# Kernel tuning notes

Hardware: AMD Instinct MI355X
Metric: run time of the kernel (lower is better)

The kernel has to match this reference:

```python
import jax, jax.numpy as jnp
import numpy as np

B, V, N, H, C_OUT = 16, 8192, 2048, 128, 7


def setup_inputs() -> dict:
    key = jax.random.key(0)
    ks = jax.random.split(key, 5)
    return {
        "verts": jax.random.normal(ks[0], (B, V, 3), jnp.float32) * 10.0,
        "coords_ca": jax.random.normal(ks[1], (B, N, 3), jnp.float32) * 10.0,
        "feats": jax.random.normal(ks[2], (B, N, H), jnp.float32),
        "W1": jax.random.normal(ks[3], (H, H), jnp.float32) / np.sqrt(H),
        "b1": jnp.zeros((H,), jnp.float32),
        "W2": jax.random.normal(ks[4], (H, C_OUT), jnp.float32) / np.sqrt(H),
        "b2": jnp.zeros((C_OUT,), jnp.float32),
    }


def reference(verts, coords_ca, feats, W1, b1, W2, b2):
    # Per-graph: nearest-CA match for every surface vertex (cdist + argmin),
    # then sum over the UNIQUE set of matched residues (torch: processed[min_indices.unique()].sum(-2)).
    # Equivalent jit-friendly form: hit-mask over residues, masked sum.
    def per_graph(v, c, f):
        # squared euclidean distances [V, N]; argmin is invariant to the sqrt
        d = (jnp.sum(v * v, -1)[:, None]
             - 2.0 * (v @ c.T)
             + jnp.sum(c * c, -1)[None, :])
        mi = jnp.argmin(d, axis=1)                       # [V] nearest residue per vertex
        hit = jnp.zeros((c.shape[0],), f.dtype).at[mi].add(1.0)
        mask = (hit > 0).astype(f.dtype)                 # [N] residue selected at least once
        return jnp.einsum('nh,n->h', f, mask)            # sum over unique selected residues

    pooled = jax.vmap(per_graph)(verts, coords_ca, feats)  # [B, H]
    # top_net (Dropout is identity in eval)
    h = jax.nn.relu(pooled @ W1 + b1)
    return h @ W2 + b2                                    # [B, 7]
```

## Files before the change

kernel.cpp:

```cpp
#include <hip/hip_runtime.h>
#include <hip/hip_bf16.h>

#define B_GR   16
#define V_PTS  8192
#define N_RES  2048
#define H_DIM  128
#define C_OUT  7
#define SEGS   16

#define NSPLIT 16
#define NL     (N_RES / NSPLIT)
#define VPT    8
#define VBLK   (256 * VPT)
#define VBLKS  (V_PTS / VBLK)

__global__ __launch_bounds__(256, 4) void k_argmin(const float* __restrict__ verts,
                                                   const float* __restrict__ coords,
                                                   unsigned long long* __restrict__ mi64) {
    __shared__ float4 sc[NL];
    const int b  = blockIdx.x / (VBLKS * NSPLIT);
    const int r  = blockIdx.x % (VBLKS * NSPLIT);
    const int vb = r / NSPLIT;
    const int ns = r % NSPLIT;

    const float* cbase = coords + ((size_t)b * N_RES + ns * NL) * 3;
    if (threadIdx.x < NL) {
        const int i = threadIdx.x;
        float x = cbase[i * 3 + 0];
        float y = cbase[i * 3 + 1];
        float z = cbase[i * 3 + 2];
        float csq = __fadd_rn(__fadd_rn(__fmul_rn(x, x), __fmul_rn(y, y)), __fmul_rn(z, z));
        sc[i] = make_float4(x, y, z, csq);
    }
    __syncthreads();

    const int vbase = vb * VBLK + threadIdx.x;
    const float* vp = verts + (size_t)b * V_PTS * 3;

    float vx[VPT], vy[VPT], vz[VPT], vsq[VPT], best[VPT];
    int bi[VPT];
#pragma unroll
    for (int k = 0; k < VPT; ++k) {
        const int v = vbase + k * 256;
        vx[k] = vp[v * 3 + 0];
        vy[k] = vp[v * 3 + 1];
        vz[k] = vp[v * 3 + 2];
        vsq[k] = __fadd_rn(__fadd_rn(__fmul_rn(vx[k], vx[k]), __fmul_rn(vy[k], vy[k])),
                           __fmul_rn(vz[k], vz[k]));
        best[k] = 3.402823466e+38f;
        bi[k] = 0;
    }

#pragma unroll 2
    for (int n = 0; n < NL; ++n) {
        const float4 c = sc[n];
#pragma unroll
        for (int k = 0; k < VPT; ++k) {
            float dot = __fadd_rn(__fadd_rn(__fmul_rn(vx[k], c.x), __fmul_rn(vy[k], c.y)),
                                  __fmul_rn(vz[k], c.z));
            float d = __fadd_rn(fmaf(-2.0f, dot, vsq[k]), c.w);
            bool m = d < best[k];
            best[k] = m ? d : best[k];
            bi[k]   = m ? n : bi[k];
        }
    }

#pragma unroll
    for (int k = 0; k < VPT; ++k) {
        unsigned int bits = __float_as_uint(best[k]);
        unsigned int key  = bits ^ (unsigned int)(((int)bits >> 31) | 0x80000000);
        unsigned long long packed =
            ((unsigned long long)key << 32) | (unsigned int)(ns * NL + bi[k]);
        atomicMin(&mi64[(size_t)b * V_PTS + vbase + k * 256], packed);
    }
}

__global__ __launch_bounds__(256) void k_pool(const unsigned long long* __restrict__ mi64,
                                              const float* __restrict__ feats,
                                              float* __restrict__ partial) {
    __shared__ float msk[N_RES];
    __shared__ float4 red[8][32];
    const int b   = blockIdx.x >> 4;
    const int seg = blockIdx.x & (SEGS - 1);

    for (int i = threadIdx.x; i < N_RES; i += 256) msk[i] = 0.0f;
    __syncthreads();

    const unsigned long long* mb = mi64 + (size_t)b * V_PTS;
    for (int v = threadIdx.x; v < V_PTS; v += 256)
        msk[(unsigned int)mb[v]] = 1.0f;
    __syncthreads();

    const int q = threadIdx.x & 31;
    const int s = threadIdx.x >> 5;
    const int n0 = seg * (N_RES / SEGS);
    const float4* fb4 = (const float4*)(feats + ((size_t)b * N_RES + n0) * H_DIM);

    float4 acc = make_float4(0.f, 0.f, 0.f, 0.f);
#pragma unroll
    for (int n = 0; n < N_RES / SEGS / 8; ++n) {
        const int nn = s + n * 8;
        const float m = msk[n0 + nn];
        const float4 f = fb4[(size_t)nn * 32 + q];
        acc.x = fmaf(f.x, m, acc.x);
        acc.y = fmaf(f.y, m, acc.y);
        acc.z = fmaf(f.z, m, acc.z);
        acc.w = fmaf(f.w, m, acc.w);
    }
    red[s][q] = acc;
    __syncthreads();

    if (s == 0) {
        float4 t = acc;
#pragma unroll
        for (int i = 1; i < 8; ++i) {
            t.x += red[i][q].x; t.y += red[i][q].y;
            t.z += red[i][q].z; t.w += red[i][q].w;
        }
        ((float4*)partial)[((size_t)b * SEGS + seg) * 32 + q] = t;
    }
}

__global__ __launch_bounds__(128) void k_mlp(const float* __restrict__ partial,
                                             const float* __restrict__ W1,
                                             const float* __restrict__ b1,
                                             const float* __restrict__ W2,
                                             const float* __restrict__ b2,
                                             float* __restrict__ out) {
    __shared__ float pooled[H_DIM];
    __shared__ float h1[H_DIM];
    const int b = blockIdx.x;
    const int j = threadIdx.x;

    float s = 0.0f;
#pragma unroll
    for (int g = 0; g < SEGS; ++g)
        s += partial[((size_t)b * SEGS + g) * H_DIM + j];
    pooled[j] = s;
    __syncthreads();

    float acc = b1[j];
#pragma unroll 8
    for (int hh = 0; hh < H_DIM; ++hh)
        acc = fmaf(pooled[hh], W1[hh * H_DIM + j], acc);
    h1[j] = fmaxf(acc, 0.0f);
    __syncthreads();

    if (j < C_OUT) {
        float o = b2[j];
#pragma unroll 8
        for (int hh = 0; hh < H_DIM; ++hh)
            o = fmaf(h1[hh], W2[hh * C_OUT + j], o);
        out[(size_t)b * C_OUT + j] = o;
    }
}

extern "C" void kernel_launch(void* const* d_in, const int* in_sizes, int n_in,
                              void* d_out, int out_size, void* d_ws, size_t ws_size,
                              hipStream_t stream) {
    const float* verts  = (const float*)d_in[0];
    const float* coords = (const float*)d_in[1];
    const float* feats  = (const float*)d_in[2];
    const float* W1     = (const float*)d_in[3];
    const float* b1     = (const float*)d_in[4];
    const float* W2     = (const float*)d_in[5];
    const float* b2     = (const float*)d_in[6];
    float* out = (float*)d_out;

    unsigned long long* mi64 = (unsigned long long*)d_ws;
    float* partial = (float*)((char*)d_ws + (size_t)B_GR * V_PTS * 8);

    hipMemsetAsync(mi64, 0xFF, (size_t)B_GR * V_PTS * 8, stream);
    k_argmin<<<B_GR * VBLKS * NSPLIT, 256, 0, stream>>>(verts, coords, mi64);
    k_pool  <<<B_GR * SEGS,           256, 0, stream>>>(mi64, feats, partial);
    k_mlp   <<<B_GR,                  128, 0, stream>>>(partial, W1, b1, W2, b2, out);
}
```

Baseline: 150.8 us.

## Use packed FP32 math in argmin and fuse pooling with MLP via last-block counter

The argmin inner loop now works on pairs of vertices using v_pk_mul/add/fma_f32 inline asm, halving the VALU instruction count for the distance computation while keeping the separate rounding of the unfused reference. The pool and MLP kernels are merged: each pooling block increments a per-graph global counter, and the last block to finish reads all partials and runs the MLP. This removes one kernel launch, at the cost of a threadfence and an atomic per block, and relies on the counter resetting itself correctly between calls.

```diff
diff --git a/kernel.cpp b/kernel.cpp
--- a/kernel.cpp
+++ b/kernel.cpp
@@ -11,8 +11,13 @@
 #define NSPLIT 16
 #define NL     (N_RES / NSPLIT)
 #define VPT    8
+#define NP     (VPT / 2)
 #define VBLK   (256 * VPT)
 #define VBLKS  (V_PTS / VBLK)
+
+typedef float f32x2 __attribute__((ext_vector_type(2)));
+
+__device__ unsigned int g_cnt[B_GR];
 
 __global__ __launch_bounds__(256, 4) void k_argmin(const float* __restrict__ verts,
                                                    const float* __restrict__ coords,
@@ -37,31 +42,61 @@
     const int vbase = vb * VBLK + threadIdx.x;
     const float* vp = verts + (size_t)b * V_PTS * 3;
 
-    float vx[VPT], vy[VPT], vz[VPT], vsq[VPT], best[VPT];
+    f32x2 vx2[NP], vy2[NP], vz2[NP], vq2[NP];
+    float best[VPT];
     int bi[VPT];
 #pragma unroll
-    for (int k = 0; k < VPT; ++k) {
-        const int v = vbase + k * 256;
-        vx[k] = vp[v * 3 + 0];
-        vy[k] = vp[v * 3 + 1];
-        vz[k] = vp[v * 3 + 2];
-        vsq[k] = __fadd_rn(__fadd_rn(__fmul_rn(vx[k], vx[k]), __fmul_rn(vy[k], vy[k])),
-                           __fmul_rn(vz[k], vz[k]));
-        best[k] = 3.402823466e+38f;
-        bi[k] = 0;
-    }
+    for (int j = 0; j < NP; ++j) {
+#pragma unroll
+        for (int h = 0; h < 2; ++h) {
+            const int k = 2 * j + h;
+            const int v = vbase + k * 256;
+            float x = vp[v * 3 + 0];
+            float y = vp[v * 3 + 1];
+            float z = vp[v * 3 + 2];
+            vx2[j][h] = x;
+            vy2[j][h] = y;
+            vz2[j][h] = z;
+            vq2[j][h] = __fadd_rn(__fadd_rn(__fmul_rn(x, x), __fmul_rn(y, y)),
+                                  __fmul_rn(z, z));
+            best[k] = 3.402823466e+38f;
+            bi[k] = 0;
+        }
+    }
+
+    const f32x2 neg2 = {-2.0f, -2.0f};
 
 #pragma unroll 2
     for (int n = 0; n < NL; ++n) {
         const float4 c = sc[n];
-#pragma unroll
-        for (int k = 0; k < VPT; ++k) {
-            float dot = __fadd_rn(__fadd_rn(__fmul_rn(vx[k], c.x), __fmul_rn(vy[k], c.y)),
-                                  __fmul_rn(vz[k], c.z));
-            float d = __fadd_rn(fmaf(-2.0f, dot, vsq[k]), c.w);
-            bool m = d < best[k];
-            best[k] = m ? d : best[k];
-            bi[k]   = m ? n : bi[k];
+        f32x2 cxy, czw;
+        cxy.x = c.x; cxy.y = c.y;
+        czw.x = c.z; czw.y = c.w;
+#pragma unroll
+        for (int j = 0; j < NP; ++j) {
+            f32x2 m0, m1, m2, s0, dot, e, d;
+            asm("v_pk_mul_f32 %0, %1, %2 op_sel:[0,0] op_sel_hi:[1,0]"
+                : "=v"(m0) : "v"(vx2[j]), "v"(cxy));
+            asm("v_pk_mul_f32 %0, %1, %2 op_sel:[0,1] op_sel_hi:[1,1]"
+                : "=v"(m1) : "v"(vy2[j]), "v"(cxy));
+            asm("v_pk_add_f32 %0, %1, %2"
+                : "=v"(s0) : "v"(m0), "v"(m1));
+            asm("v_pk_mul_f32 %0, %1, %2 op_sel:[0,0] op_sel_hi:[1,0]"
+                : "=v"(m2) : "v"(vz2[j]), "v"(czw));
+            asm("v_pk_add_f32 %0, %1, %2"
+                : "=v"(dot) : "v"(s0), "v"(m2));
+            asm("v_pk_fma_f32 %0, %1, %2, %3"
+                : "=v"(e) : "v"(neg2), "v"(dot), "v"(vq2[j]));
+            asm("v_pk_add_f32 %0, %1, %2 op_sel:[0,1] op_sel_hi:[1,1]"
+                : "=v"(d) : "v"(e), "v"(czw));
+
+            const int k0 = 2 * j, k1 = 2 * j + 1;
+            bool mlo = d.x < best[k0];
+            best[k0] = mlo ? d.x : best[k0];
+            bi[k0]   = mlo ? n : bi[k0];
+            bool mhi = d.y < best[k1];
+            best[k1] = mhi ? d.y : best[k1];
+            bi[k1]   = mhi ? n : bi[k1];
         }
     }
 
@@ -75,11 +110,19 @@
     }
 }
 
-__global__ __launch_bounds__(256) void k_pool(const unsigned long long* __restrict__ mi64,
-                                              const float* __restrict__ feats,
-                                              float* __restrict__ partial) {
+__global__ __launch_bounds__(256) void k_pool_mlp(const unsigned long long* __restrict__ mi64,
+                                                  const float* __restrict__ feats,
+                                                  const float* __restrict__ W1,
+                                                  const float* __restrict__ b1,
+                                                  const float* __restrict__ W2,
+                                                  const float* __restrict__ b2,
+                                                  float* __restrict__ partial,
+                                                  float* __restrict__ out) {
     __shared__ float msk[N_RES];
     __shared__ float4 red[8][32];
+    __shared__ unsigned int slast;
+    __shared__ float pooled[H_DIM];
+    __shared__ float h1[H_DIM];
     const int b   = blockIdx.x >> 4;
     const int seg = blockIdx.x & (SEGS - 1);
 
@@ -119,33 +162,36 @@
         }
         ((float4*)partial)[((size_t)b * SEGS + seg) * 32 + q] = t;
     }
-}
-
-__global__ __launch_bounds__(128) void k_mlp(const float* __restrict__ partial,
-                                             const float* __restrict__ W1,
-                                             const float* __restrict__ b1,
-                                             const float* __restrict__ W2,
-                                             const float* __restrict__ b2,
-                                             float* __restrict__ out) {
-    __shared__ float pooled[H_DIM];
-    __shared__ float h1[H_DIM];
-    const int b = blockIdx.x;
+
+    __threadfence();
+    __syncthreads();
+    if (threadIdx.x == 0) {
+        unsigned int old = atomicAdd(&g_cnt[b], 1u);
+        unsigned int lastf = (old == SEGS - 1) ? 1u : 0u;
+        if (lastf) g_cnt[b] = 0u;
+        slast = lastf;
+    }
+    __syncthreads();
+    if (!slast) return;
+
+    __threadfence();
     const int j = threadIdx.x;
-
-    float s = 0.0f;
-#pragma unroll
-    for (int g = 0; g < SEGS; ++g)
-        s += partial[((size_t)b * SEGS + g) * H_DIM + j];
-    pooled[j] = s;
-    __syncthreads();
-
-    float acc = b1[j];
+    if (j < H_DIM) {
+        float sum = 0.0f;
+#pragma unroll
+        for (int g = 0; g < SEGS; ++g)
+            sum += partial[((size_t)b * SEGS + g) * H_DIM + j];
+        pooled[j] = sum;
+    }
+    __syncthreads();
+    if (j < H_DIM) {
+        float a1 = b1[j];
 #pragma unroll 8
-    for (int hh = 0; hh < H_DIM; ++hh)
-        acc = fmaf(pooled[hh], W1[hh * H_DIM + j], acc);
-    h1[j] = fmaxf(acc, 0.0f);
-    __syncthreads();
-
+        for (int hh = 0; hh < H_DIM; ++hh)
+            a1 = fmaf(pooled[hh], W1[hh * H_DIM + j], a1);
+        h1[j] = fmaxf(a1, 0.0f);
+    }
+    __syncthreads();
     if (j < C_OUT) {
         float o = b2[j];
 #pragma unroll 8
@@ -171,7 +217,7 @@
     float* partial = (float*)((char*)d_ws + (size_t)B_GR * V_PTS * 8);
 
     hipMemsetAsync(mi64, 0xFF, (size_t)B_GR * V_PTS * 8, stream);
-    k_argmin<<<B_GR * VBLKS * NSPLIT, 256, 0, stream>>>(verts, coords, mi64);
-    k_pool  <<<B_GR * SEGS,           256, 0, stream>>>(mi64, feats, partial);
-    k_mlp   <<<B_GR,                  128, 0, stream>>>(partial, W1, b1, W2, b2, out);
+    k_argmin  <<<B_GR * VBLKS * NSPLIT, 256, 0, stream>>>(verts, coords, mi64);
+    k_pool_mlp<<<B_GR * SEGS,           256, 0, stream>>>(mi64, feats, W1, b1, W2, b2,
+                                                          partial, out);
 }
```

After: 173.5 us. 15.0% more time.

## Replace 64-bit atomicMin argmin merge with per-split stores and merge kernel

Applied to the files above, without the earlier changes.

The argmin kernel now writes each split's packed (distance, index) result to its own slot in a workspace buffer instead of doing global 64-bit atomicMin. A new merge kernel reduces the 16 splits per vertex and scatters the hit mask directly to global memory. The pool kernel then reads a precomputed mask slice rather than having every block rebuild the full mask from all vertices. This is meant to remove atomic contention and the redundant per-block mask construction, but it adds an extra launch and about 16 MB of extra workspace traffic. When the workspace is too small, the code falls back to the old atomic path.

```diff
diff --git a/kernel.cpp b/kernel.cpp
--- a/kernel.cpp
+++ b/kernel.cpp
@@ -14,9 +14,9 @@
 #define VBLK   (256 * VPT)
 #define VBLKS  (V_PTS / VBLK)
 
-__global__ __launch_bounds__(256, 4) void k_argmin(const float* __restrict__ verts,
-                                                   const float* __restrict__ coords,
-                                                   unsigned long long* __restrict__ mi64) {
+__global__ __launch_bounds__(256, 4) void k_argmin_st(const float* __restrict__ verts,
+                                                      const float* __restrict__ coords,
+                                                      unsigned long long* __restrict__ part) {
     __shared__ float4 sc[NL];
     const int b  = blockIdx.x / (VBLKS * NSPLIT);
     const int r  = blockIdx.x % (VBLKS * NSPLIT);
@@ -65,6 +65,126 @@
         }
     }
 
+    unsigned long long* op = part + ((size_t)(b * NSPLIT + ns)) * V_PTS + vbase;
+#pragma unroll
+    for (int k = 0; k < VPT; ++k) {
+        unsigned int bits = __float_as_uint(best[k]);
+        unsigned int key  = bits ^ (unsigned int)(((int)bits >> 31) | 0x80000000);
+        unsigned long long packed =
+            ((unsigned long long)key << 32) | (unsigned int)(ns * NL + bi[k]);
+        op[k * 256] = packed;
+    }
+}
+
+__global__ __launch_bounds__(256) void k_merge(const unsigned long long* __restrict__ part,
+                                               float* __restrict__ msk) {
+    const int gv = blockIdx.x * 256 + threadIdx.x;
+    const int b  = gv >> 13;
+    const int v  = gv & (V_PTS - 1);
+
+    const unsigned long long* p = part + (size_t)b * NSPLIT * V_PTS + v;
+    unsigned long long c[NSPLIT];
+#pragma unroll
+    for (int s = 0; s < NSPLIT; ++s)
+        c[s] = p[(size_t)s * V_PTS];
+    unsigned long long best = c[0];
+#pragma unroll
+    for (int s = 1; s < NSPLIT; ++s)
+        best = c[s] < best ? c[s] : best;
+
+    msk[b * N_RES + (unsigned int)best] = 1.0f;
+}
+
+__global__ __launch_bounds__(256) void k_pool_m(const float* __restrict__ msk,
+                                                const float* __restrict__ feats,
+                                                float* __restrict__ partial) {
+    __shared__ float sm[NL];
+    __shared__ float4 red[8][32];
+    const int b   = blockIdx.x >> 4;
+    const int seg = blockIdx.x & (SEGS - 1);
+    const int n0  = seg * (N_RES / SEGS);
+
+    if (threadIdx.x < NL) sm[threadIdx.x] = msk[b * N_RES + n0 + threadIdx.x];
+    __syncthreads();
+
+    const int q = threadIdx.x & 31;
+    const int s = threadIdx.x >> 5;
+    const float4* fb4 = (const float4*)(feats + ((size_t)b * N_RES + n0) * H_DIM);
+
+    float4 acc = make_float4(0.f, 0.f, 0.f, 0.f);
+#pragma unroll
+    for (int n = 0; n < N_RES / SEGS / 8; ++n) {
+        const int nn = s + n * 8;
+        const float m = sm[nn];
+        const float4 f = fb4[(size_t)nn * 32 + q];
+        acc.x = fmaf(f.x, m, acc.x);
+        acc.y = fmaf(f.y, m, acc.y);
+        acc.z = fmaf(f.z, m, acc.z);
+        acc.w = fmaf(f.w, m, acc.w);
+    }
+    red[s][q] = acc;
+    __syncthreads();
+
+    if (s == 0) {
+        float4 t = acc;
+#pragma unroll
+        for (int i = 1; i < 8; ++i) {
+            t.x += red[i][q].x; t.y += red[i][q].y;
+            t.z += red[i][q].z; t.w += red[i][q].w;
+        }
+        ((float4*)partial)[((size_t)b * SEGS + seg) * 32 + q] = t;
+    }
+}
+
+__global__ __launch_bounds__(256, 4) void k_argmin_at(const float* __restrict__ verts,
+                                                      const float* __restrict__ coords,
+                                                      unsigned long long* __restrict__ mi64) {
+    __shared__ float4 sc[NL];
+    const int b  = blockIdx.x / (VBLKS * NSPLIT);
+    const int r  = blockIdx.x % (VBLKS * NSPLIT);
+    const int vb = r / NSPLIT;
+    const int ns = r % NSPLIT;
+
+    const float* cbase = coords + ((size_t)b * N_RES + ns * NL) * 3;
+    if (threadIdx.x < NL) {
+        const int i = threadIdx.x;
+        float x = cbase[i * 3 + 0];
+        float y = cbase[i * 3 + 1];
+        float z = cbase[i * 3 + 2];
+        float csq = __fadd_rn(__fadd_rn(__fmul_rn(x, x), __fmul_rn(y, y)), __fmul_rn(z, z));
+        sc[i] = make_float4(x, y, z, csq);
+    }
+    __syncthreads();
+
+    const int vbase = vb * VBLK + threadIdx.x;
+    const float* vp = verts + (size_t)b * V_PTS * 3;
+
+    float vx[VPT], vy[VPT], vz[VPT], vsq[VPT], best[VPT];
+    int bi[VPT];
+#pragma unroll
+    for (int k = 0; k < VPT; ++k) {
+        const int v = vbase + k * 256;
+        vx[k] = vp[v * 3 + 0];
+        vy[k] = vp[v * 3 + 1];
+        vz[k] = vp[v * 3 + 2];
+        vsq[k] = __fadd_rn(__fadd_rn(__fmul_rn(vx[k], vx[k]), __fmul_rn(vy[k], vy[k])),
+                           __fmul_rn(vz[k], vz[k]));
+        best[k] = 3.402823466e+38f;
+        bi[k] = 0;
+    }
+#pragma unroll 2
+    for (int n = 0; n < NL; ++n) {
+        const float4 c = sc[n];
+#pragma unroll
+        for (int k = 0; k < VPT; ++k) {
+            float dot = __fadd_rn(__fadd_rn(__fmul_rn(vx[k], c.x), __fmul_rn(vy[k], c.y)),
+                                  __fmul_rn(vz[k], c.z));
+            float d = __fadd_rn(fmaf(-2.0f, dot, vsq[k]), c.w);
+            bool m = d < best[k];
+            best[k] = m ? d : best[k];
+            bi[k]   = m ? n : bi[k];
+        }
+    }
 #pragma unroll
     for (int k = 0; k < VPT; ++k) {
         unsigned int bits = __float_as_uint(best[k]);
@@ -75,9 +195,9 @@
     }
 }
 
-__global__ __launch_bounds__(256) void k_pool(const unsigned long long* __restrict__ mi64,
-                                              const float* __restrict__ feats,
-                                              float* __restrict__ partial) {
+__global__ __launch_bounds__(256) void k_pool_at(const unsigned long long* __restrict__ mi64,
+                                                 const float* __restrict__ feats,
+                                                 float* __restrict__ partial) {
     __shared__ float msk[N_RES];
     __shared__ float4 red[8][32];
     const int b   = blockIdx.x >> 4;
@@ -85,7 +205,6 @@
 
     for (int i = threadIdx.x; i < N_RES; i += 256) msk[i] = 0.0f;
     __syncthreads();
-
     const unsigned long long* mb = mi64 + (size_t)b * V_PTS;
     for (int v = threadIdx.x; v < V_PTS; v += 256)
         msk[(unsigned int)mb[v]] = 1.0f;
@@ -109,7 +228,6 @@
     }
     red[s][q] = acc;
     __syncthreads();
-
     if (s == 0) {
         float4 t = acc;
 #pragma unroll
@@ -167,11 +285,27 @@
     const float* b2     = (const float*)d_in[6];
     float* out = (float*)d_out;
 
-    unsigned long long* mi64 = (unsigned long long*)d_ws;
-    float* partial = (float*)((char*)d_ws + (size_t)B_GR * V_PTS * 8);
-
-    hipMemsetAsync(mi64, 0xFF, (size_t)B_GR * V_PTS * 8, stream);
-    k_argmin<<<B_GR * VBLKS * NSPLIT, 256, 0, stream>>>(verts, coords, mi64);
-    k_pool  <<<B_GR * SEGS,           256, 0, stream>>>(mi64, feats, partial);
-    k_mlp   <<<B_GR,                  128, 0, stream>>>(partial, W1, b1, W2, b2, out);
-}
+    const size_t part_bytes = (size_t)B_GR * NSPLIT * V_PTS * 8;
+    const size_t msk_bytes  = (size_t)B_GR * N_RES * 4;
+    const size_t pp_bytes   = (size_t)B_GR * SEGS * H_DIM * 4;
+
+    if (ws_size >= part_bytes + msk_bytes + pp_bytes) {
+        unsigned long long* part = (unsigned long long*)d_ws;
+        float* msk     = (float*)((char*)d_ws + part_bytes);
+        float* partial = (float*)((char*)d_ws + part_bytes + msk_bytes);
+
+        hipMemsetAsync(msk, 0, msk_bytes, stream);
+        k_argmin_st<<<B_GR * VBLKS * NSPLIT, 256, 0, stream>>>(verts, coords, part);
+        k_merge    <<<B_GR * V_PTS / 256,    256, 0, stream>>>(part, msk);
+        k_pool_m   <<<B_GR * SEGS,           256, 0, stream>>>(msk, feats, partial);
+        k_mlp      <<<B_GR,                  128, 0, stream>>>(partial, W1, b1, W2, b2, out);
+    } else {
+        unsigned long long* mi64 = (unsigned long long*)d_ws;
+        float* partial = (float*)((char*)d_ws + (size_t)B_GR * V_PTS * 8);
+
+        hipMemsetAsync(mi64, 0xFF, (size_t)B_GR * V_PTS * 8, stream);
+        k_argmin_at<<<B_GR * VBLKS * NSPLIT, 256, 0, stream>>>(verts, coords, mi64);
+        k_pool_at  <<<B_GR * SEGS,           256, 0, stream>>>(mi64, feats, partial);
+        k_mlp      <<<B_GR,                  128, 0, stream>>>(partial, W1, b1, W2, b2, out);
+    }
+}
```

Result: faster. 146.4 us (-3.0%).
